# Kernel tuning notes

Measured on AMD Instinct MI355X. Metric: run time of the kernel, lower is better.

The kernel has to match this reference:

```python
import jax, jax.numpy as jnp
import numpy as np

BETA = 0.95      # LIF membrane decay (init arg)
THR = 1.0        # snntorch Leaky default threshold
NUM_STEPS = 128


@jax.custom_vjp
def spike(x):
    # Heaviside fire with ATan surrogate gradient (snntorch default, alpha=2)
    return (x > 0).astype(x.dtype)

def _spike_fwd(x):
    return spike(x), x

def _spike_bwd(x, g):
    return (g / (1.0 + (jnp.pi * x) ** 2),)

spike.defvjp(_spike_fwd, _spike_bwd)


def setup_inputs() -> dict:
    key = jax.random.key(0)
    ks = jax.random.split(key, 5)
    B, NI, NH, NO = 2048, 1024, 2048, 10
    return {
        "x": jax.random.normal(ks[0], (B, NI), dtype=jnp.float32),
        "w1": jax.random.normal(ks[1], (NH, NI), dtype=jnp.float32) * 0.05,
        "b1": jax.random.normal(ks[2], (NH,), dtype=jnp.float32) * 0.05,
        "w2": jax.random.normal(ks[3], (NO, NH), dtype=jnp.float32) * 0.05,
        "b2": jax.random.normal(ks[4], (NO,), dtype=jnp.float32) * 0.05,
    }


def reference(x, w1, b1, w2, b2):
    # fc1(x) is loop-invariant: compute the input current once.
    cur1 = jnp.einsum("bi,hi->bh", x, w1) + b1  # [B, NH]
    mem1_0 = jnp.zeros_like(cur1)
    mem2_0 = jnp.zeros((x.shape[0], w2.shape[0]), dtype=x.dtype)

    def step(carry, _):
        mem1, mem2 = carry
        # snntorch Leaky, reset-by-subtraction; reset term is detached.
        reset1 = jax.lax.stop_gradient((mem1 > THR).astype(mem1.dtype))
        mem1 = BETA * mem1 + cur1 - reset1 * THR
        spk1 = spike(mem1 - THR)
        cur2 = jnp.einsum("bh,oh->bo", spk1, w2) + b2  # [B, NO]
        reset2 = jax.lax.stop_gradient((mem2 > THR).astype(mem2.dtype))
        mem2 = BETA * mem2 + cur2 - reset2 * THR
        spk2 = spike(mem2 - THR)
        return (mem1, mem2), (spk2, mem2)

    _, (spk2_rec, mem2_rec) = jax.lax.scan(step, (mem1_0, mem2_0), None, length=NUM_STEPS)
    return spk2_rec, mem2_rec  # each [T, B, NO]
```

## Files before the change

### kernel.cpp

```cpp
#include <hip/hip_runtime.h>
#include <hip/hip_bf16.h>


#define B_   2048
#define NI_  1024
#define NH_  2048
#define NO_  10
#define T_   128
#define GB_  8
#define NBLK (B_ / GB_)
#define TC_  32
#define NCH  (T_ / TC_)

typedef __attribute__((ext_vector_type(8))) short short8;
typedef __attribute__((ext_vector_type(4))) float f32x4;
typedef __attribute__((ext_vector_type(4))) unsigned int u32x4;

__device__ __forceinline__ unsigned int bf16_rne(float f) {
  unsigned int u = __float_as_uint(f);
  return (u + 0x7FFFu + ((u >> 16) & 1u)) >> 16;
}

#define G_ASTRIDE 144
#define G_AOFF    0
#define G_BOFF    (128 * G_ASTRIDE)
#define G_SMEM    (2 * 128 * G_ASTRIDE)

__global__ __launch_bounds__(512, 2) void gemm_cur1(
    const float* __restrict__ x, const float* __restrict__ w1,
    const float* __restrict__ b1, float* __restrict__ cur1) {
  __shared__ __align__(16) char smem[G_SMEM];
  const int tid = threadIdx.x;
  const int lane = tid & 63;
  const int wv = tid >> 6;
  const int wm = wv >> 2;
  const int wn = wv & 3;
  const int n15 = lane & 15;
  const int g = lane >> 4;
  const int brow = blockIdx.y * 128;
  const int bcol = blockIdx.x * 128;

  const int r_st = tid >> 3;
  const int kq = tid & 7;

  f32x4 acc[4][2];
#pragma unroll
  for (int tm = 0; tm < 4; ++tm)
#pragma unroll
    for (int tn = 0; tn < 2; ++tn) acc[tm][tn] = f32x4{0, 0, 0, 0};

  for (int kt = 0; kt < NI_; kt += 32) {
#pragma unroll
    for (int p = 0; p < 2; ++p) {
      const int r = r_st + p * 64;
      const float4 va = *reinterpret_cast<const float4*>(
          &x[(size_t)(brow + r) * NI_ + kt + kq * 4]);
      const float4 vb = *reinterpret_cast<const float4*>(
          &w1[(size_t)(bcol + r) * NI_ + kt + kq * 4]);
      const float fa[4] = {va.x, va.y, va.z, va.w};
      const float fb[4] = {vb.x, vb.y, vb.z, vb.w};
      unsigned ha[4], la[4], hb[4], lb[4];
#pragma unroll
      for (int c = 0; c < 4; ++c) {
        ha[c] = bf16_rne(fa[c]);
        la[c] = bf16_rne(fa[c] - __uint_as_float(ha[c] << 16));
        hb[c] = bf16_rne(fb[c]);
        lb[c] = bf16_rne(fb[c] - __uint_as_float(hb[c] << 16));
      }
      char* arow = smem + G_AOFF + r * G_ASTRIDE;
      char* brw  = smem + G_BOFF + r * G_ASTRIDE;
      *reinterpret_cast<uint2*>(arow + kq * 8) =
          uint2{ha[0] | (ha[1] << 16), ha[2] | (ha[3] << 16)};
      *reinterpret_cast<uint2*>(arow + 64 + kq * 8) =
          uint2{la[0] | (la[1] << 16), la[2] | (la[3] << 16)};
      *reinterpret_cast<uint2*>(brw + kq * 8) =
          uint2{hb[0] | (hb[1] << 16), hb[2] | (hb[3] << 16)};
      *reinterpret_cast<uint2*>(brw + 64 + kq * 8) =
          uint2{lb[0] | (lb[1] << 16), lb[2] | (lb[3] << 16)};
    }
    __syncthreads();

    short8 ah[4], al[4], bh2[2], bl2[2];
#pragma unroll
    for (int tm = 0; tm < 4; ++tm) {
      const char* p = smem + G_AOFF + (wm * 64 + tm * 16 + n15) * G_ASTRIDE;
      ah[tm] = *reinterpret_cast<const short8*>(p + g * 16);
      al[tm] = *reinterpret_cast<const short8*>(p + 64 + g * 16);
    }
#pragma unroll
    for (int tn = 0; tn < 2; ++tn) {
      const char* p = smem + G_BOFF + (wn * 32 + tn * 16 + n15) * G_ASTRIDE;
      bh2[tn] = *reinterpret_cast<const short8*>(p + g * 16);
      bl2[tn] = *reinterpret_cast<const short8*>(p + 64 + g * 16);
    }
#pragma unroll
    for (int tm = 0; tm < 4; ++tm)
#pragma unroll
      for (int tn = 0; tn < 2; ++tn) {
        acc[tm][tn] = __builtin_amdgcn_mfma_f32_16x16x32_bf16(
            ah[tm], bh2[tn], acc[tm][tn], 0, 0, 0);
        acc[tm][tn] = __builtin_amdgcn_mfma_f32_16x16x32_bf16(
            ah[tm], bl2[tn], acc[tm][tn], 0, 0, 0);
        acc[tm][tn] = __builtin_amdgcn_mfma_f32_16x16x32_bf16(
            al[tm], bh2[tn], acc[tm][tn], 0, 0, 0);
      }
    __syncthreads();
  }

#pragma unroll
  for (int tn = 0; tn < 2; ++tn) {
    const int col = bcol + wn * 32 + tn * 16 + n15;
    const float bias = b1[col];
#pragma unroll
    for (int tm = 0; tm < 4; ++tm) {
      const int rowb = brow + wm * 64 + tm * 16 + g * 4;
#pragma unroll
      for (int r = 0; r < 4; ++r)
        cur1[(size_t)(rowb + r) * NH_ + col] = acc[tm][tn][r] + bias;
    }
  }
}

#define LUT_OFF  0
#define BITS_OFF 4096
#define COMB_OFF 70656
#define SMEM_BYTES 152576

__global__ __launch_bounds__(512, 2) void snn_loop(
    const float* __restrict__ cur1, const float* __restrict__ w2,
    const float* __restrict__ b2, float* __restrict__ spk2_rec,
    float* __restrict__ mem2_rec) {
  extern __shared__ char smem[];
  unsigned* bits = reinterpret_cast<unsigned*>(smem + BITS_OFF);
  float* comb = reinterpret_cast<float*>(smem + COMB_OFF);
  const int tid = threadIdx.x;
  const int lane = tid & 63;
  const int w = tid >> 6;
  const int bbase = blockIdx.x * GB_;
  const int bb = bbase + w;

  if (tid < 256) {
    u32x4 e;
#pragma unroll
    for (int q = 0; q < 4; ++q)
      e[q] = ((tid >> (2 * q)) & 1 ? 0x3F80u : 0u) |
             ((tid >> (2 * q + 1)) & 1 ? 0x3F800000u : 0u);
    *reinterpret_cast<u32x4*>(smem + LUT_OFF + tid * 16) = e;
  }

  float mem1[32], c1v[32], c1m[32], cc[32];
  {
    const float* base = cur1 + (size_t)bb * NH_ + lane * 32;
#pragma unroll
    for (int q = 0; q < 8; ++q) {
      const float4 v = *reinterpret_cast<const float4*>(base + q * 4);
      c1v[q * 4 + 0] = v.x; c1v[q * 4 + 1] = v.y;
      c1v[q * 4 + 2] = v.z; c1v[q * 4 + 3] = v.w;
    }
#pragma unroll
    for (int i = 0; i < 32; ++i) {
      mem1[i] = 0.0f;
      c1m[i] = c1v[i] - 1.0f;
      cc[i] = c1v[i];
    }
  }

  u32x4 bhi[8], blo[8];
  {
    const int o = lane & 15;
    const int koff = (lane >> 4) * 8;
#pragma unroll
    for (int kbl = 0; kbl < 8; ++kbl) {
      const int kb = w * 8 + kbl;
      unsigned int hw[4], lw[4];
#pragma unroll
      for (int p = 0; p < 4; ++p) {
        unsigned int h0 = 0, h1 = 0, l0 = 0, l1 = 0;
        if (o < NO_) {
          const int k = kb * 32 + koff + p * 2;
          const float f0 = w2[(size_t)o * NH_ + k];
          const float f1 = w2[(size_t)o * NH_ + k + 1];
          h0 = bf16_rne(f0);
          h1 = bf16_rne(f1);
          l0 = bf16_rne(f0 - __uint_as_float(h0 << 16));
          l1 = bf16_rne(f1 - __uint_as_float(h1 << 16));
        }
        hw[p] = h0 | (h1 << 16);
        lw[p] = l0 | (l1 << 16);
      }
      bhi[kbl] = u32x4{hw[0], hw[1], hw[2], hw[3]};
      blo[kbl] = u32x4{lw[0], lw[1], lw[2], lw[3]};
    }
  }

  float mem2 = 0.0f, spk2 = 0.0f, b2v = 0.0f;
  float *srec = nullptr, *mrec = nullptr;
  if (lane < NO_) {
    b2v = b2[lane];
    srec = spk2_rec + (size_t)bb * NO_ + lane;
    mrec = mem2_rec + (size_t)bb * NO_ + lane;
  }

  const int n15 = lane & 15;
  const int g = lane >> 4;

  unsigned* bitsrow = bits + w * 2080 + lane;
  const int base_bg = BITS_OFF + n15 * 260 + w * 32 + g;
  const unsigned char* bytes = reinterpret_cast<const unsigned char*>(smem);

  for (int ch = 0; ch < NCH; ++ch) {
    for (int tl = 0; tl < TC_; ++tl) {
      unsigned W = 0;
#pragma unroll
      for (int i = 31; i >= 0; --i) {
        const float m = fmaf(0.95f, mem1[i], cc[i]);
        mem1[i] = m;
        const bool c = m > 1.0f;
        W = W + W + (c ? 1u : 0u);
        cc[i] = c ? c1m[i] : c1v[i];
      }
      bitsrow[tl * 65] = W;
    }
    __syncthreads();

    for (int b = 0; b < GB_; ++b) {
#pragma unroll
      for (int tb = 0; tb < 2; ++tb) {
        const int rbase = base_bg + b * 8320 + tb * 4160;
        f32x4 acc = {0.0f, 0.0f, 0.0f, 0.0f};
#pragma unroll
        for (int kbl = 0; kbl < 8; ++kbl) {
          const unsigned byt = bytes[rbase + kbl * 4];
          const short8 af = *reinterpret_cast<const short8*>(
              smem + LUT_OFF + (byt << 4));
          acc = __builtin_amdgcn_mfma_f32_16x16x32_bf16(
              af, __builtin_bit_cast(short8, bhi[kbl]), acc, 0, 0, 0);
          acc = __builtin_amdgcn_mfma_f32_16x16x32_bf16(
              af, __builtin_bit_cast(short8, blo[kbl]), acc, 0, 0, 0);
        }
        if (n15 < NO_)
          *reinterpret_cast<f32x4*>(
              &comb[w * 2560 + b * 320 + tb * 160 + g * 40 + n15 * 4]) = acc;
      }
    }
    __syncthreads();

    if (lane < NO_) {
      const float* cbase = comb + w * 320 + lane * 4;
#pragma unroll
      for (int tl = 0; tl < TC_; ++tl) {
        const int off = (tl >> 4) * 160 + ((tl & 15) >> 2) * 40 + (tl & 3);
        float s = 0.0f;
#pragma unroll
        for (int ww = 0; ww < 8; ++ww) s += cbase[ww * 2560 + off];
        const float cur2 = s + b2v;
        float m = fmaf(0.95f, mem2, cur2);
        m = m - spk2;
        mem2 = m;
        spk2 = (m > 1.0f) ? 1.0f : 0.0f;
        const int t = ch * TC_ + tl;
        srec[(size_t)t * (B_ * NO_)] = spk2;
        mrec[(size_t)t * (B_ * NO_)] = m;
      }
    }
  }
}

extern "C" void kernel_launch(void* const* d_in, const int* in_sizes, int n_in,
                              void* d_out, int out_size, void* d_ws, size_t ws_size,
                              hipStream_t stream) {
  const float* x  = (const float*)d_in[0];
  const float* w1 = (const float*)d_in[1];
  const float* b1 = (const float*)d_in[2];
  const float* w2 = (const float*)d_in[3];
  const float* b2 = (const float*)d_in[4];
  float* out = (float*)d_out;
  float* cur1 = (float*)d_ws;

  float* spk2_rec = out;
  float* mem2_rec = out + (size_t)T_ * B_ * NO_;

  (void)hipFuncSetAttribute(reinterpret_cast<const void*>(snn_loop),
                            hipFuncAttributeMaxDynamicSharedMemorySize,
                            SMEM_BYTES);

  dim3 g1(NH_ / 128, B_ / 128);
  gemm_cur1<<<g1, 512, 0, stream>>>(x, w1, b1, cur1);
  snn_loop<<<NBLK, 512, SMEM_BYTES, stream>>>(cur1, w2, b2, spk2_rec, mem2_rec);
}
```

Measured before the change: 185.7 us.

## Software-pipeline SNN loop with double-buffered spike bits and partial sums

Restructures the time loop so the layer-1 membrane update for the next chunk of timesteps is interleaved with the MFMA layer-2 products for the current chunk. Bits and combine buffers are double-buffered, and the serial mem2 recurrence runs one chunk behind, which removes one barrier per chunk. The chunk size is halved and the 4 KB byte-to-bf16 LUT is replaced by a 16-entry nibble LUT that builds each A fragment from two small loads. The cost is more LDS lookups per MFMA, extra register pressure from the interleaved code, and a prologue/epilogue.

```diff
diff --git a/kernel.cpp b/kernel.cpp
--- a/kernel.cpp
+++ b/kernel.cpp
@@ -9,7 +9,7 @@
 #define T_   128
 #define GB_  8
 #define NBLK (B_ / GB_)
-#define TC_  32
+#define TC_  16
 #define NCH  (T_ / TC_)
 
 typedef __attribute__((ext_vector_type(8))) short short8;
@@ -122,15 +122,19 @@
 }
 
 #define LUT_OFF  0
-#define BITS_OFF 4096
-#define COMB_OFF 70656
-#define SMEM_BYTES 152576
+#define BITS_OFF 128
+#define BITS_PAR 8320
+#define COMB_OFF 66688
+#define COMB_PAR 10240
+#define SMEM_BYTES 148608
 
 __global__ __launch_bounds__(512, 2) void snn_loop(
     const float* __restrict__ cur1, const float* __restrict__ w2,
     const float* __restrict__ b2, float* __restrict__ spk2_rec,
     float* __restrict__ mem2_rec) {
   extern __shared__ char smem[];
+  uint2* lutw = reinterpret_cast<uint2*>(smem + LUT_OFF);
+  const uint2* lut = lutw;
   unsigned* bits = reinterpret_cast<unsigned*>(smem + BITS_OFF);
   float* comb = reinterpret_cast<float*>(smem + COMB_OFF);
   const int tid = threadIdx.x;
@@ -139,13 +143,9 @@
   const int bbase = blockIdx.x * GB_;
   const int bb = bbase + w;
 
-  if (tid < 256) {
-    u32x4 e;
-#pragma unroll
-    for (int q = 0; q < 4; ++q)
-      e[q] = ((tid >> (2 * q)) & 1 ? 0x3F80u : 0u) |
-             ((tid >> (2 * q + 1)) & 1 ? 0x3F800000u : 0u);
-    *reinterpret_cast<u32x4*>(smem + LUT_OFF + tid * 16) = e;
+  if (tid < 16) {
+    lutw[tid] = uint2{(tid & 1 ? 0x3F80u : 0u) | (tid & 2 ? 0x3F800000u : 0u),
+                      (tid & 4 ? 0x3F80u : 0u) | (tid & 8 ? 0x3F800000u : 0u)};
   }
 
   float mem1[32], c1v[32], c1m[32], cc[32];
@@ -203,65 +203,94 @@
 
   const int n15 = lane & 15;
   const int g = lane >> 4;
-
-  unsigned* bitsrow = bits + w * 2080 + lane;
-  const int base_bg = BITS_OFF + n15 * 260 + w * 32 + g;
   const unsigned char* bytes = reinterpret_cast<const unsigned char*>(smem);
 
+  auto P1_STEP = [&](unsigned* bitsP, int tl) {
+    unsigned W = 0;
+#pragma unroll
+    for (int i = 31; i >= 0; --i) {
+      const float m = fmaf(0.95f, mem1[i], cc[i]);
+      mem1[i] = m;
+      const bool c = m > 1.0f;
+      W = W + W + (c ? 1u : 0u);
+      cc[i] = c ? c1m[i] : c1v[i];
+    }
+    bitsP[(w * TC_ + tl) * 65 + lane] = W;
+  };
+
+  for (int tl = 0; tl < TC_; ++tl) P1_STEP(bits, tl);
+  __syncthreads();
+
   for (int ch = 0; ch < NCH; ++ch) {
-    for (int tl = 0; tl < TC_; ++tl) {
-      unsigned W = 0;
-#pragma unroll
-      for (int i = 31; i >= 0; --i) {
-        const float m = fmaf(0.95f, mem1[i], cc[i]);
-        mem1[i] = m;
-        const bool c = m > 1.0f;
-        W = W + W + (c ? 1u : 0u);
-        cc[i] = c ? c1m[i] : c1v[i];
-      }
-      bitsrow[tl * 65] = W;
-    }
-    __syncthreads();
-
-    for (int b = 0; b < GB_; ++b) {
-#pragma unroll
-      for (int tb = 0; tb < 2; ++tb) {
-        const int rbase = base_bg + b * 8320 + tb * 4160;
-        f32x4 acc = {0.0f, 0.0f, 0.0f, 0.0f};
-#pragma unroll
-        for (int kbl = 0; kbl < 8; ++kbl) {
-          const unsigned byt = bytes[rbase + kbl * 4];
-          const short8 af = *reinterpret_cast<const short8*>(
-              smem + LUT_OFF + (byt << 4));
-          acc = __builtin_amdgcn_mfma_f32_16x16x32_bf16(
-              af, __builtin_bit_cast(short8, bhi[kbl]), acc, 0, 0, 0);
-          acc = __builtin_amdgcn_mfma_f32_16x16x32_bf16(
-              af, __builtin_bit_cast(short8, blo[kbl]), acc, 0, 0, 0);
-        }
-        if (n15 < NO_)
-          *reinterpret_cast<f32x4*>(
-              &comb[w * 2560 + b * 320 + tb * 160 + g * 40 + n15 * 4]) = acc;
-      }
-    }
-    __syncthreads();
-
-    if (lane < NO_) {
-      const float* cbase = comb + w * 320 + lane * 4;
+    const int cur = ch & 1;
+    unsigned* bitsN = bits + (cur ^ 1) * BITS_PAR;
+    float* combC = comb + cur * COMB_PAR;
+    const float* combV = comb + (cur ^ 1) * COMB_PAR;
+    const int bbyte = BITS_OFF + cur * (BITS_PAR * 4);
+
+    if (ch > 0 && lane < NO_) {
+      const float* cbase = combV + w * 160 + lane * 4;
 #pragma unroll
       for (int tl = 0; tl < TC_; ++tl) {
-        const int off = (tl >> 4) * 160 + ((tl & 15) >> 2) * 40 + (tl & 3);
+        const int off = (tl >> 2) * 40 + (tl & 3);
         float s = 0.0f;
 #pragma unroll
-        for (int ww = 0; ww < 8; ++ww) s += cbase[ww * 2560 + off];
+        for (int ww = 0; ww < 8; ++ww) s += cbase[ww * 1280 + off];
         const float cur2 = s + b2v;
         float m = fmaf(0.95f, mem2, cur2);
         m = m - spk2;
         mem2 = m;
         spk2 = (m > 1.0f) ? 1.0f : 0.0f;
-        const int t = ch * TC_ + tl;
+        const int t = (ch - 1) * TC_ + tl;
         srec[(size_t)t * (B_ * NO_)] = spk2;
         mrec[(size_t)t * (B_ * NO_)] = m;
       }
+    }
+
+#pragma unroll
+    for (int b = 0; b < GB_; ++b) {
+      const int rbase = bbyte + ((b * TC_ + n15) * 65 + w * 8) * 4 + g;
+      f32x4 acc = {0.0f, 0.0f, 0.0f, 0.0f};
+#pragma unroll
+      for (int kbl = 0; kbl < 8; ++kbl) {
+        const unsigned byt = bytes[rbase + kbl * 4];
+        const uint2 lo2 = lut[byt & 15u];
+        const uint2 hi2 = lut[byt >> 4];
+        const u32x4 A = {lo2.x, lo2.y, hi2.x, hi2.y};
+        const short8 af = __builtin_bit_cast(short8, A);
+        acc = __builtin_amdgcn_mfma_f32_16x16x32_bf16(
+            af, __builtin_bit_cast(short8, bhi[kbl]), acc, 0, 0, 0);
+        acc = __builtin_amdgcn_mfma_f32_16x16x32_bf16(
+            af, __builtin_bit_cast(short8, blo[kbl]), acc, 0, 0, 0);
+      }
+      if (n15 < NO_)
+        *reinterpret_cast<f32x4*>(
+            &combC[w * 1280 + b * 160 + g * 40 + n15 * 4]) = acc;
+      if (ch < NCH - 1) {
+        P1_STEP(bitsN, 2 * b);
+        P1_STEP(bitsN, 2 * b + 1);
+      }
+    }
+
+    __syncthreads();
+  }
+
+  if (lane < NO_) {
+    const float* cbase = comb + ((NCH - 1) & 1) * COMB_PAR + w * 160 + lane * 4;
+#pragma unroll
+    for (int tl = 0; tl < TC_; ++tl) {
+      const int off = (tl >> 2) * 40 + (tl & 3);
+      float s = 0.0f;
+#pragma unroll
+      for (int ww = 0; ww < 8; ++ww) s += cbase[ww * 1280 + off];
+      const float cur2 = s + b2v;
+      float m = fmaf(0.95f, mem2, cur2);
+      m = m - spk2;
+      mem2 = m;
+      spk2 = (m > 1.0f) ? 1.0f : 0.0f;
+      const int t = (NCH - 1) * TC_ + tl;
+      srec[(size_t)t * (B_ * NO_)] = spk2;
+      mrec[(size_t)t * (B_ * NO_)] = m;
     }
   }
 }
```

Result: faster. 181.0 us (-2.5%).
